# Performance work log

Hardware: AMD Instinct MI355X
Metric: run time of the kernel (lower is better)

Reference implementation:

```python
import jax, jax.numpy as jnp
import numpy as np

B, T, I, D = 64, 512, 512, 512


def hard_sigmoid(x):
    return jnp.clip(0.2 * x + 0.5, 0.0, 1.0)


def setup_inputs() -> dict:
    key = jax.random.key(0)
    ks = jax.random.split(key, 8)
    u = lambda k, sh: jax.random.uniform(k, sh, jnp.float32, -0.05, 0.05)  # keras 'uniform'
    gn = lambda k, sh: jax.random.normal(k, sh, jnp.float32) * jnp.sqrt(2.0 / (sh[0] + sh[1]))  # glorot_normal
    return {
        "X": jax.random.normal(ks[0], (B, T, I), jnp.float32),
        "W": u(ks[1], (I, D)),
        "b": jnp.zeros((D,), jnp.float32),
        "W_in": u(ks[2], (I, D)),
        "b_in": jnp.zeros((D,), jnp.float32),
        "W_out": u(ks[3], (I, D)),
        "b_out": jnp.zeros((D,), jnp.float32),
        "U": gn(ks[4], (D, D)),
        "U_in": gn(ks[5], (D, D)),
        "U_out": gn(ks[6], (D, D)),
        "bu_in": jnp.zeros((D,), jnp.float32),
        "bu_out": jnp.zeros((D,), jnp.float32),
    }


def reference(X, W, b, W_in, b_in, W_out, b_out, U, U_in, U_out, bu_in, bu_out):
    Xt = jnp.swapaxes(X, 0, 1)            # (T, B, I)
    xx = Xt @ W + b                       # (T, B, D) input projections (done once)
    x_in = Xt @ W_in + b_in
    x_out = Xt @ W_out + b_out
    # theano scan with sequence taps [-1,-2]: step t uses proj[t] and proj[t-1], t = 1..T-1
    seqs = (xx[1:], xx[:-1], x_in[1:], x_in[:-1], x_out[1:], x_out[:-1])

    def step(h, s):
        a, a_m1, p, p_m1, q, q_m1 = s
        z = hard_sigmoid(a + h @ U + a_m1)
        z_in = hard_sigmoid(p + h @ U_in + p_m1 + bu_in)
        z_out = jax.nn.softplus(q + (z_in * h) @ U_out + q_m1 + bu_out)
        h_t = (1.0 - z) * h + z * z_out
        return h_t, None

    h0 = jnp.zeros((X.shape[0], U.shape[0]), X.dtype)  # initial h_{-1} = 0
    h_last, _ = jax.lax.scan(step, h0, seqs)
    return h_last  # return_sequences=False -> last hidden state, (B, D)
```

## Files before the change

kernel.cpp:

```cpp
#include <hip/hip_runtime.h>
#include <hip/hip_bf16.h>


typedef __attribute__((ext_vector_type(4))) float  f32x4;
typedef __attribute__((ext_vector_type(4))) float  floatx4;
typedef __attribute__((ext_vector_type(8))) short  short8;
typedef __attribute__((ext_vector_type(4))) short  short4v;
typedef __attribute__((ext_vector_type(2))) int    int2v;

#define NSTEP  511
#define NGRP   4
#define NCOLB  32
#define NAN_S  ((short)0x7FFF)

#define OFF_HB0  4096
#define OFF_HB1  (OFF_HB0 + 65536)
#define OFF_GB0  (OFF_HB1 + 65536)
#define OFF_GB1  (OFF_GB0 + 65536)
#define OFF_HF32 (OFF_GB1 + 65536)
#define OFF_UPK  (OFF_HF32 + 131072)
#define OFF_WT   (OFF_UPK + 1572864)
#define OFF_XX   (OFF_WT + 1572864)
#define PER_T_BYTES (3u * 64u * 512u * 2u)

__device__ __forceinline__ float b2f(short s) {
  unsigned u = ((unsigned)(unsigned short)s) << 16;
  return __builtin_bit_cast(float, u);
}
__device__ __forceinline__ short f2b(float f) {
  unsigned u = __builtin_bit_cast(unsigned, f);
  u += 0x7fffu + ((u >> 16) & 1u);
  return (short)(u >> 16);
}
__device__ __forceinline__ float hsig(float x) {
  return fminf(fmaxf(0.2f * x + 0.5f, 0.0f), 1.0f);
}
__device__ __forceinline__ float softplus_f(float x) {
  return fmaxf(x, 0.0f) + log1pf(expf(-fabsf(x)));
}

__device__ __forceinline__ void st8_cp(short* p, int2v v) {
  asm volatile("global_store_dwordx2 %0, %1, off sc0 sc1"
               :: "v"(p), "v"(v) : "memory");
}

__device__ __forceinline__ void ld_frags16(const short* p0, const short* p1,
                                           const short* p2, const short* p3,
                                           short8 f[16]) {
  short8 f0,f1,f2,f3,f4,f5,f6,f7,f8,f9,f10,f11,f12,f13,f14,f15;
  asm volatile(
    "global_load_dwordx4 %0,  %16, off sc0 sc1\n\t"
    "global_load_dwordx4 %1,  %16, off offset:1024 sc0 sc1\n\t"
    "global_load_dwordx4 %2,  %16, off offset:2048 sc0 sc1\n\t"
    "global_load_dwordx4 %3,  %16, off offset:3072 sc0 sc1\n\t"
    "global_load_dwordx4 %4,  %17, off sc0 sc1\n\t"
    "global_load_dwordx4 %5,  %17, off offset:1024 sc0 sc1\n\t"
    "global_load_dwordx4 %6,  %17, off offset:2048 sc0 sc1\n\t"
    "global_load_dwordx4 %7,  %17, off offset:3072 sc0 sc1\n\t"
    "global_load_dwordx4 %8,  %18, off sc0 sc1\n\t"
    "global_load_dwordx4 %9,  %18, off offset:1024 sc0 sc1\n\t"
    "global_load_dwordx4 %10, %18, off offset:2048 sc0 sc1\n\t"
    "global_load_dwordx4 %11, %18, off offset:3072 sc0 sc1\n\t"
    "global_load_dwordx4 %12, %19, off sc0 sc1\n\t"
    "global_load_dwordx4 %13, %19, off offset:1024 sc0 sc1\n\t"
    "global_load_dwordx4 %14, %19, off offset:2048 sc0 sc1\n\t"
    "global_load_dwordx4 %15, %19, off offset:3072 sc0 sc1\n\t"
    "s_waitcnt vmcnt(0)"
    : "=&v"(f0), "=&v"(f1), "=&v"(f2), "=&v"(f3),
      "=&v"(f4), "=&v"(f5), "=&v"(f6), "=&v"(f7),
      "=&v"(f8), "=&v"(f9), "=&v"(f10), "=&v"(f11),
      "=&v"(f12), "=&v"(f13), "=&v"(f14), "=&v"(f15)
    : "v"(p0), "v"(p1), "v"(p2), "v"(p3)
    : "memory");
  f[0]=f0; f[1]=f1; f[2]=f2; f[3]=f3; f[4]=f4; f[5]=f5; f[6]=f6; f[7]=f7;
  f[8]=f8; f[9]=f9; f[10]=f10; f[11]=f11; f[12]=f12; f[13]=f13; f[14]=f14; f[15]=f15;
}

__device__ __forceinline__ void poll_frags16(const short* base, short8 f[16]) {
  const short* q0 = base;
  const short* q1 = base + 2048;
  const short* q2 = base + 4096;
  const short* q3 = base + 6144;
  int guard = 0;
  for (;;) {
    ld_frags16(q0, q1, q2, q3, f);
    int fresh = 1;
    #pragma unroll
    for (int i = 0; i < 16; ++i)
      fresh &= (f[i][0] != NAN_S) & (f[i][4] != NAN_S);
    if (__all(fresh)) break;
    if (++guard > (1 << 13)) break;
  }
}

__global__ __launch_bounds__(256) void prep_kernel(
    const float* __restrict__ U0, const float* __restrict__ U1, const float* __restrict__ U2,
    const float* __restrict__ W0, const float* __restrict__ W1, const float* __restrict__ W2,
    short* __restrict__ Upk, short* __restrict__ Wt)
{
  int e = blockIdx.x * 256 + threadIdx.x;
  if (e < 786432) {
    int mat = e >> 18;
    int rem = e & 262143;
    int c   = rem >> 13;
    int r2  = rem & 8191;
    int kb  = r2 >> 9;
    int r3  = r2 & 511;
    int l = r3 >> 3, j = r3 & 7;
    int k = kb * 32 + ((l >> 4) << 3) + j;
    int d = c * 16 + (l & 15);
    const float* U = (mat == 0) ? U0 : (mat == 1 ? U1 : U2);
    Upk[e] = f2b(U[k * 512 + d]);
  } else if (e < 1572864) {
    int e2 = e - 786432;
    int mat = e2 >> 18;
    int rem = e2 & 262143;
    int n = rem >> 9, k = rem & 511;
    const float* W = (mat == 0) ? W0 : (mat == 1 ? W1 : W2);
    Wt[e2] = f2b(W[k * 512 + n]);
  }
}

__global__ __launch_bounds__(256) void init_kernel(
    short* hb0, short* hb1, short* gb0, short* gb1, float* h_f32)
{
  int e = blockIdx.x * 256 + threadIdx.x;
  if (e < 32768) {
    hb0[e] = NAN_S; hb1[e] = 0;
    gb0[e] = NAN_S; gb1[e] = NAN_S;
    h_f32[e] = 0.0f;
  }
}

__global__ __launch_bounds__(256) void gemm_xw(
    const float* __restrict__ X, const short* __restrict__ Wt,
    const float* __restrict__ bias0, const float* __restrict__ bias1,
    const float* __restrict__ bias2, short* __restrict__ out,
    int base_row, int cnt_rows)
{
  __shared__ __align__(16) short Al[128][48];
  __shared__ __align__(16) short Bl[128][48];
  const int bm = blockIdx.x, bn = blockIdx.y, mat = blockIdx.z;
  const short* Wm = Wt + (size_t)mat * (512 * 512);
  const float* bias = (mat == 0) ? bias0 : (mat == 1 ? bias1 : bias2);
  short* om = out + (size_t)mat * ((size_t)cnt_rows * 512);
  const int tid = threadIdx.x, lane = tid & 63, wid = tid >> 6;
  const int wm = wid >> 1, wn = wid & 1;
  const int m0 = bm * 128, n0g = bn * 128;
  f32x4 acc[4][4];
  #pragma unroll
  for (int i = 0; i < 4; ++i)
    #pragma unroll
    for (int j = 0; j < 4; ++j) acc[i][j] = (f32x4){0.f, 0.f, 0.f, 0.f};

  for (int k0 = 0; k0 < 512; k0 += 32) {
    #pragma unroll
    for (int i = 0; i < 4; ++i) {
      int q = tid + 256 * i;
      int r = q >> 3, seg = q & 7;
      int ml = m0 + r;
      short4v h4 = {0, 0, 0, 0};
      if (ml < cnt_rows) {
        int gl = base_row + ml;
        int t = gl >> 6, bb = gl & 63;
        floatx4 v = *(const floatx4*)(X + ((size_t)bb * 512 + t) * 512 + k0 + seg * 4);
        h4 = (short4v){ f2b(v[0]), f2b(v[1]), f2b(v[2]), f2b(v[3]) };
      }
      *(short4v*)&Al[r][seg * 4] = h4;
    }
    #pragma unroll
    for (int i = 0; i < 2; ++i) {
      int q = tid + 256 * i;
      int r = q >> 2, seg = q & 3;
      *(short8*)&Bl[r][seg * 8] = *(const short8*)(Wm + (size_t)(n0g + r) * 512 + k0 + seg * 8);
    }
    __syncthreads();
    const int ko = (lane >> 4) * 8;
    short8 af[4], bf4[4];
    #pragma unroll
    for (int mt = 0; mt < 4; ++mt)
      af[mt] = *(const short8*)&Al[wm * 64 + mt * 16 + (lane & 15)][ko];
    #pragma unroll
    for (int nt = 0; nt < 4; ++nt)
      bf4[nt] = *(const short8*)&Bl[wn * 64 + nt * 16 + (lane & 15)][ko];
    #pragma unroll
    for (int mt = 0; mt < 4; ++mt)
      #pragma unroll
      for (int nt = 0; nt < 4; ++nt)
        acc[mt][nt] = __builtin_amdgcn_mfma_f32_16x16x32_bf16(af[mt], bf4[nt], acc[mt][nt], 0, 0, 0);
    __syncthreads();
  }
  const int rq = lane >> 4, cq = lane & 15;
  #pragma unroll
  for (int mt = 0; mt < 4; ++mt) {
    #pragma unroll
    for (int nt = 0; nt < 4; ++nt) {
      int n = n0g + wn * 64 + nt * 16 + cq;
      float bv = bias[n];
      #pragma unroll
      for (int rr = 0; rr < 4; ++rr) {
        int m = m0 + wm * 64 + mt * 16 + rq * 4 + rr;
        if (m < cnt_rows) om[(size_t)m * 512 + n] = f2b(acc[mt][nt][rr] + bv);
      }
    }
  }
}

__global__ __launch_bounds__(64, 1) void scan_kernel(
    short* hb0, short* hb1, short* gb0, short* gb1, float* h_f32,
    const short* __restrict__ Upk,
    const short* __restrict__ xx,
    const float* __restrict__ bu_in, const float* __restrict__ bu_out,
    float* __restrict__ out,
    int s0, int nsteps, int nt)
{
  __shared__ __align__(16) short Ub[3][16][64][8];
  __shared__ __align__(16) short St[256];
  const int lane = threadIdx.x & 63;
  const int g = blockIdx.x >> 5;
  const int c = blockIdx.x & 31;
  {
    const size_t cs = (size_t)c * 8192;
    short8* dst = (short8*)Ub;
    for (int i = lane; i < 3072; i += 64) {
      int mat = i >> 10;
      int rem = i & 1023;
      dst[i] = *(const short8*)(Upk + (size_t)mat * 262144 + cs + (size_t)rem * 8);
    }
  }
  const int colg = c * 16 + (lane & 15);
  const float binr  = bu_in[colg];
  const float boutr = bu_out[colg];
  const size_t XSZ = (size_t)nt * 64 * 512;
  const int gbase = g * 8192;
  const int fofs = gbase + ((lane >> 4) << 7) + ((lane & 15) << 3);
  const int pofs = gbase + ((c >> 1) << 9) + ((c & 1) << 8) + (lane << 2);
  const int sw = ((lane & 15) >> 3) * 128 + ((lane >> 4) << 5) + (lane & 7);
  short* hbuf[2] = { hb0, hb1 };
  short* gbuf[2] = { gb0, gb1 };
  const int2v NANPAIR = { 0x7FFF7FFF, 0x7FFF7FFF };

  float hown[4];
  #pragma unroll
  for (int r = 0; r < 4; ++r)
    hown[r] = h_f32[(size_t)(g * 16 + (lane >> 4) * 4 + r) * 512 + colg];
  __syncthreads();

  for (int s = 0; s < nsteps; ++s) {
    const int sg = s0 + s;
    const int p = sg & 1;
    float a1[4], a0[4], p1[4], p0[4], q1[4], q0[4];
    #pragma unroll
    for (int r = 0; r < 4; ++r) {
      int gr = g * 16 + (lane >> 4) * 4 + r;
      size_t i1 = ((size_t)(s + 1) * 64 + gr) * 512 + colg;
      size_t i0 = ((size_t)s * 64 + gr) * 512 + colg;
      a1[r] = b2f(xx[i1]);           a0[r] = b2f(xx[i0]);
      p1[r] = b2f(xx[XSZ + i1]);     p0[r] = b2f(xx[XSZ + i0]);
      q1[r] = b2f(xx[2 * XSZ + i1]); q0[r] = b2f(xx[2 * XSZ + i0]);
    }

    short8 afr[16];
    poll_frags16(hbuf[p ^ 1] + fofs, afr);
    if (sg > 0) st8_cp(gbuf[p ^ 1] + pofs, NANPAIR);

    f32x4 ai[4];
    ai[0] = ai[1] = ai[2] = ai[3] = (f32x4){0.f, 0.f, 0.f, 0.f};
    #pragma unroll
    for (int kb = 0; kb < 16; ++kb) {
      short8 b1 = *((const short8*)Ub + ((1 * 16 + kb) * 64 + lane));
      ai[kb & 3] = __builtin_amdgcn_mfma_f32_16x16x32_bf16(afr[kb], b1, ai[kb & 3], 0, 0, 0);
    }
    f32x4 accin = (ai[0] + ai[1]) + (ai[2] + ai[3]);
    #pragma unroll
    for (int r = 0; r < 4; ++r) {
      float zin = hsig(p1[r] + accin[r] + p0[r] + binr);
      St[sw + r * 8] = f2b(zin * hown[r]);
    }
    st8_cp(gbuf[p] + pofs, *(const int2v*)&St[lane << 2]);

    f32x4 au[4];
    au[0] = au[1] = au[2] = au[3] = (f32x4){0.f, 0.f, 0.f, 0.f};
    #pragma unroll
    for (int kb = 0; kb < 16; ++kb) {
      short8 b0 = *((const short8*)Ub + ((0 * 16 + kb) * 64 + lane));
      au[kb & 3] = __builtin_amdgcn_mfma_f32_16x16x32_bf16(afr[kb], b0, au[kb & 3], 0, 0, 0);
    }
    f32x4 accu = (au[0] + au[1]) + (au[2] + au[3]);
    float zr[4];
    #pragma unroll
    for (int r = 0; r < 4; ++r)
      zr[r] = hsig(a1[r] + accu[r] + a0[r]);

    short8 gfr[16];
    poll_frags16(gbuf[p] + fofs, gfr);
    st8_cp(hbuf[p ^ 1] + pofs, NANPAIR);
    f32x4 ao[4];
    ao[0] = ao[1] = ao[2] = ao[3] = (f32x4){0.f, 0.f, 0.f, 0.f};
    #pragma unroll
    for (int kb = 0; kb < 16; ++kb) {
      short8 b2 = *((const short8*)Ub + ((2 * 16 + kb) * 64 + lane));
      ao[kb & 3] = __builtin_amdgcn_mfma_f32_16x16x32_bf16(gfr[kb], b2, ao[kb & 3], 0, 0, 0);
    }
    f32x4 acco = (ao[0] + ao[1]) + (ao[2] + ao[3]);
    #pragma unroll
    for (int r = 0; r < 4; ++r) {
      float pre = q1[r] + acco[r] + q0[r] + boutr;
      float zo = softplus_f(pre);
      float hn = (1.0f - zr[r]) * hown[r] + zr[r] * zo;
      hown[r] = hn;
      St[sw + r * 8] = f2b(hn);
    }
    st8_cp(hbuf[p] + pofs, *(const int2v*)&St[lane << 2]);
    if (sg == NSTEP - 1) {
      #pragma unroll
      for (int r = 0; r < 4; ++r) {
        int gr = g * 16 + (lane >> 4) * 4 + r;
        out[(size_t)gr * 512 + colg] = hown[r];
      }
    }
  }
  #pragma unroll
  for (int r = 0; r < 4; ++r)
    h_f32[(size_t)(g * 16 + (lane >> 4) * 4 + r) * 512 + colg] = hown[r];
  asm volatile("s_waitcnt vmcnt(0)" ::: "memory");
}

extern "C" void kernel_launch(void* const* d_in, const int* in_sizes, int n_in,
                              void* d_out, int out_size, void* d_ws, size_t ws_size,
                              hipStream_t stream)
{
  const float* X      = (const float*)d_in[0];
  const float* W      = (const float*)d_in[1];
  const float* b      = (const float*)d_in[2];
  const float* W_in   = (const float*)d_in[3];
  const float* b_in   = (const float*)d_in[4];
  const float* W_out  = (const float*)d_in[5];
  const float* b_out  = (const float*)d_in[6];
  const float* U      = (const float*)d_in[7];
  const float* U_in   = (const float*)d_in[8];
  const float* U_out  = (const float*)d_in[9];
  const float* bu_in  = (const float*)d_in[10];
  const float* bu_out = (const float*)d_in[11];
  float* out = (float*)d_out;
  char* ws = (char*)d_ws;
  short* hb0  = (short*)(ws + OFF_HB0);
  short* hb1  = (short*)(ws + OFF_HB1);
  short* gb0  = (short*)(ws + OFF_GB0);
  short* gb1  = (short*)(ws + OFF_GB1);
  float* h_f32= (float*)(ws + OFF_HF32);
  short* Upk  = (short*)(ws + OFF_UPK);
  short* Wt   = (short*)(ws + OFF_WT);
  short* xx   = (short*)(ws + OFF_XX);

  size_t avail = (ws_size > (size_t)OFF_XX) ? ws_size - (size_t)OFF_XX : 0;
  int max_t = (int)(avail / PER_T_BYTES);
  if (max_t > 512) max_t = 512;
  int SEG = max_t - 1;
  if (SEG < 1) SEG = 1;

  prep_kernel<<<6144, 256, 0, stream>>>(U, U_in, U_out, W, W_in, W_out, Upk, Wt);
  init_kernel<<<128, 256, 0, stream>>>(hb0, hb1, gb0, gb1, h_f32);

  int s0 = 0;
  while (s0 < NSTEP) {
    int nsteps = NSTEP - s0; if (nsteps > SEG) nsteps = SEG;
    int nt = nsteps + 1;
    int rows = nt * 64;
    int gx = (rows + 127) / 128;
    gemm_xw<<<dim3(gx, 4, 3), 256, 0, stream>>>(X, Wt, b, b_in, b_out, xx,
                                                s0 * 64, rows);
    scan_kernel<<<NGRP * NCOLB, 64, 0, stream>>>(hb0, hb1, gb0, gb1, h_f32,
                                                 Upk, xx, bu_in, bu_out, out,
                                                 s0, nsteps, nt);
    s0 += nsteps;
  }
}
```

Measured before the change: 2.657 ms.

## Consume fresh h/g fragments incrementally while double-buffered polls stay in flight

Replaces the all-or-nothing polling loop, which waited until all 16 fragments were non-NaN before any MFMA, with a per-fragment freshness mask. Each fragment is fed into the MFMAs as soon as it is seen to be fresh, while the next poll load is already issued into a second register buffer. The U and U_in products are also fused into one pass over the h fragments. The aim is to overlap the cross-block synchronisation latency with matrix work, at the cost of many more registers, branchy code and a possibly different accumulation order.

```diff
diff --git a/kernel.cpp b/kernel.cpp
--- a/kernel.cpp
+++ b/kernel.cpp
@@ -44,10 +44,13 @@
                :: "v"(p), "v"(v) : "memory");
 }
 
-__device__ __forceinline__ void ld_frags16(const short* p0, const short* p1,
+struct Frags {
+  short8 f0,f1,f2,f3,f4,f5,f6,f7,f8,f9,f10,f11,f12,f13,f14,f15;
+};
+
+__device__ __forceinline__ void ld_issue16(const short* p0, const short* p1,
                                            const short* p2, const short* p3,
-                                           short8 f[16]) {
-  short8 f0,f1,f2,f3,f4,f5,f6,f7,f8,f9,f10,f11,f12,f13,f14,f15;
+                                           Frags& F) {
   asm volatile(
     "global_load_dwordx4 %0,  %16, off sc0 sc1\n\t"
     "global_load_dwordx4 %1,  %16, off offset:1024 sc0 sc1\n\t"
@@ -64,34 +67,65 @@
     "global_load_dwordx4 %12, %19, off sc0 sc1\n\t"
     "global_load_dwordx4 %13, %19, off offset:1024 sc0 sc1\n\t"
     "global_load_dwordx4 %14, %19, off offset:2048 sc0 sc1\n\t"
-    "global_load_dwordx4 %15, %19, off offset:3072 sc0 sc1\n\t"
-    "s_waitcnt vmcnt(0)"
-    : "=&v"(f0), "=&v"(f1), "=&v"(f2), "=&v"(f3),
-      "=&v"(f4), "=&v"(f5), "=&v"(f6), "=&v"(f7),
-      "=&v"(f8), "=&v"(f9), "=&v"(f10), "=&v"(f11),
-      "=&v"(f12), "=&v"(f13), "=&v"(f14), "=&v"(f15)
+    "global_load_dwordx4 %15, %19, off offset:3072 sc0 sc1"
+    : "=&v"(F.f0), "=&v"(F.f1), "=&v"(F.f2), "=&v"(F.f3),
+      "=&v"(F.f4), "=&v"(F.f5), "=&v"(F.f6), "=&v"(F.f7),
+      "=&v"(F.f8), "=&v"(F.f9), "=&v"(F.f10), "=&v"(F.f11),
+      "=&v"(F.f12), "=&v"(F.f13), "=&v"(F.f14), "=&v"(F.f15)
     : "v"(p0), "v"(p1), "v"(p2), "v"(p3)
     : "memory");
-  f[0]=f0; f[1]=f1; f[2]=f2; f[3]=f3; f[4]=f4; f[5]=f5; f[6]=f6; f[7]=f7;
-  f[8]=f8; f[9]=f9; f[10]=f10; f[11]=f11; f[12]=f12; f[13]=f13; f[14]=f14; f[15]=f15;
-}
-
-__device__ __forceinline__ void poll_frags16(const short* base, short8 f[16]) {
-  const short* q0 = base;
-  const short* q1 = base + 2048;
-  const short* q2 = base + 4096;
-  const short* q3 = base + 6144;
-  int guard = 0;
-  for (;;) {
-    ld_frags16(q0, q1, q2, q3, f);
-    int fresh = 1;
-    #pragma unroll
-    for (int i = 0; i < 16; ++i)
-      fresh &= (f[i][0] != NAN_S) & (f[i][4] != NAN_S);
-    if (__all(fresh)) break;
-    if (++guard > (1 << 13)) break;
-  }
-}
+}
+
+__device__ __forceinline__ void vmw(Frags& F) {
+  asm volatile("s_waitcnt vmcnt(0)"
+    : "+v"(F.f0), "+v"(F.f1), "+v"(F.f2), "+v"(F.f3),
+      "+v"(F.f4), "+v"(F.f5), "+v"(F.f6), "+v"(F.f7),
+      "+v"(F.f8), "+v"(F.f9), "+v"(F.f10), "+v"(F.f11),
+      "+v"(F.f12), "+v"(F.f13), "+v"(F.f14), "+v"(F.f15)
+    :: "memory");
+}
+
+#define FRESHBIT(F, i) \
+  (((unsigned)__all(((F).f##i[0] != NAN_S) & ((F).f##i[4] != NAN_S))) << i)
+
+__device__ __forceinline__ unsigned freshmask_impl(const Frags& F) {
+  unsigned m = 0;
+  m |= FRESHBIT(F, 0);  m |= FRESHBIT(F, 1);  m |= FRESHBIT(F, 2);
+  m |= FRESHBIT(F, 3);  m |= FRESHBIT(F, 4);  m |= FRESHBIT(F, 5);
+  m |= FRESHBIT(F, 6);  m |= FRESHBIT(F, 7);  m |= FRESHBIT(F, 8);
+  m |= FRESHBIT(F, 9);  m |= FRESHBIT(F, 10); m |= FRESHBIT(F, 11);
+  m |= FRESHBIT(F, 12); m |= FRESHBIT(F, 13); m |= FRESHBIT(F, 14);
+  m |= FRESHBIT(F, 15);
+  return m;
+}
+
+#define MF(a, b, c) __builtin_amdgcn_mfma_f32_16x16x32_bf16(a, b, c, 0, 0, 0)
+
+#define CONS1_ONE(F, i) \
+  if ((fr >> i) & 1) { \
+    short8 b0 = *((const short8*)Ub + ((0 * 16 + i) * 64 + lane)); \
+    short8 b1 = *((const short8*)Ub + ((1 * 16 + i) * 64 + lane)); \
+    au[i & 3] = MF((F).f##i, b0, au[i & 3]); \
+    ai[i & 3] = MF((F).f##i, b1, ai[i & 3]); \
+  }
+#define CONS1_ALL(F) do { \
+  CONS1_ONE(F, 0)  CONS1_ONE(F, 1)  CONS1_ONE(F, 2)  CONS1_ONE(F, 3)  \
+  CONS1_ONE(F, 4)  CONS1_ONE(F, 5)  CONS1_ONE(F, 6)  CONS1_ONE(F, 7)  \
+  CONS1_ONE(F, 8)  CONS1_ONE(F, 9)  CONS1_ONE(F, 10) CONS1_ONE(F, 11) \
+  CONS1_ONE(F, 12) CONS1_ONE(F, 13) CONS1_ONE(F, 14) CONS1_ONE(F, 15) \
+} while (0)
+
+#define CONS2_ONE(F, i) \
+  if ((fr >> i) & 1) { \
+    short8 b2 = *((const short8*)Ub + ((2 * 16 + i) * 64 + lane)); \
+    ao[i & 3] = MF((F).f##i, b2, ao[i & 3]); \
+  }
+#define CONS2_ALL(F) do { \
+  CONS2_ONE(F, 0)  CONS2_ONE(F, 1)  CONS2_ONE(F, 2)  CONS2_ONE(F, 3)  \
+  CONS2_ONE(F, 4)  CONS2_ONE(F, 5)  CONS2_ONE(F, 6)  CONS2_ONE(F, 7)  \
+  CONS2_ONE(F, 8)  CONS2_ONE(F, 9)  CONS2_ONE(F, 10) CONS2_ONE(F, 11) \
+  CONS2_ONE(F, 12) CONS2_ONE(F, 13) CONS2_ONE(F, 14) CONS2_ONE(F, 15) \
+} while (0)
 
 __global__ __launch_bounds__(256) void prep_kernel(
     const float* __restrict__ U0, const float* __restrict__ U1, const float* __restrict__ U2,
@@ -246,6 +280,8 @@
     hown[r] = h_f32[(size_t)(g * 16 + (lane >> 4) * 4 + r) * 512 + colg];
   __syncthreads();
 
+  Frags FA, FB;
+
   for (int s = 0; s < nsteps; ++s) {
     const int sg = s0 + s;
     const int p = sg & 1;
@@ -260,17 +296,33 @@
       q1[r] = b2f(xx[2 * XSZ + i1]); q0[r] = b2f(xx[2 * XSZ + i0]);
     }
 
-    short8 afr[16];
-    poll_frags16(hbuf[p ^ 1] + fofs, afr);
+    const short* hbp = hbuf[p ^ 1] + fofs;
+    f32x4 au[4], ai[4];
+    au[0] = au[1] = au[2] = au[3] = (f32x4){0.f, 0.f, 0.f, 0.f};
+    ai[0] = ai[1] = ai[2] = ai[3] = (f32x4){0.f, 0.f, 0.f, 0.f};
+    {
+      unsigned done = 0; int guard = 0;
+      ld_issue16(hbp, hbp + 2048, hbp + 4096, hbp + 6144, FA);
+      for (;;) {
+        vmw(FA);
+        unsigned fr = freshmask_impl(FA) & ~done;
+        unsigned nd = done | fr;
+        if (nd != 0xFFFFu) ld_issue16(hbp, hbp + 2048, hbp + 4096, hbp + 6144, FB);
+        CONS1_ALL(FA);
+        done = nd;
+        if (done == 0xFFFFu) break;
+        if (++guard > 4096) break;
+        vmw(FB);
+        fr = freshmask_impl(FB) & ~done;
+        nd = done | fr;
+        if (nd != 0xFFFFu) ld_issue16(hbp, hbp + 2048, hbp + 4096, hbp + 6144, FA);
+        CONS1_ALL(FB);
+        done = nd;
+        if (done == 0xFFFFu) break;
+        if (++guard > 4096) break;
+      }
+    }
     if (sg > 0) st8_cp(gbuf[p ^ 1] + pofs, NANPAIR);
-
-    f32x4 ai[4];
-    ai[0] = ai[1] = ai[2] = ai[3] = (f32x4){0.f, 0.f, 0.f, 0.f};
-    #pragma unroll
-    for (int kb = 0; kb < 16; ++kb) {
-      short8 b1 = *((const short8*)Ub + ((1 * 16 + kb) * 64 + lane));
-      ai[kb & 3] = __builtin_amdgcn_mfma_f32_16x16x32_bf16(afr[kb], b1, ai[kb & 3], 0, 0, 0);
-    }
     f32x4 accin = (ai[0] + ai[1]) + (ai[2] + ai[3]);
     #pragma unroll
     for (int r = 0; r < 4; ++r) {
@@ -278,30 +330,38 @@
       St[sw + r * 8] = f2b(zin * hown[r]);
     }
     st8_cp(gbuf[p] + pofs, *(const int2v*)&St[lane << 2]);
-
-    f32x4 au[4];
-    au[0] = au[1] = au[2] = au[3] = (f32x4){0.f, 0.f, 0.f, 0.f};
-    #pragma unroll
-    for (int kb = 0; kb < 16; ++kb) {
-      short8 b0 = *((const short8*)Ub + ((0 * 16 + kb) * 64 + lane));
-      au[kb & 3] = __builtin_amdgcn_mfma_f32_16x16x32_bf16(afr[kb], b0, au[kb & 3], 0, 0, 0);
-    }
     f32x4 accu = (au[0] + au[1]) + (au[2] + au[3]);
     float zr[4];
     #pragma unroll
     for (int r = 0; r < 4; ++r)
       zr[r] = hsig(a1[r] + accu[r] + a0[r]);
 
-    short8 gfr[16];
-    poll_frags16(gbuf[p] + fofs, gfr);
-    st8_cp(hbuf[p ^ 1] + pofs, NANPAIR);
+    const short* gbp = gbuf[p] + fofs;
     f32x4 ao[4];
     ao[0] = ao[1] = ao[2] = ao[3] = (f32x4){0.f, 0.f, 0.f, 0.f};
-    #pragma unroll
-    for (int kb = 0; kb < 16; ++kb) {
-      short8 b2 = *((const short8*)Ub + ((2 * 16 + kb) * 64 + lane));
-      ao[kb & 3] = __builtin_amdgcn_mfma_f32_16x16x32_bf16(gfr[kb], b2, ao[kb & 3], 0, 0, 0);
-    }
+    {
+      unsigned done = 0; int guard = 0;
+      ld_issue16(gbp, gbp + 2048, gbp + 4096, gbp + 6144, FA);
+      for (;;) {
+        vmw(FA);
+        unsigned fr = freshmask_impl(FA) & ~done;
+        unsigned nd = done | fr;
+        if (nd != 0xFFFFu) ld_issue16(gbp, gbp + 2048, gbp + 4096, gbp + 6144, FB);
+        CONS2_ALL(FA);
+        done = nd;
+        if (done == 0xFFFFu) break;
+        if (++guard > 4096) break;
+        vmw(FB);
+        fr = freshmask_impl(FB) & ~done;
+        nd = done | fr;
+        if (nd != 0xFFFFu) ld_issue16(gbp, gbp + 2048, gbp + 4096, gbp + 6144, FA);
+        CONS2_ALL(FB);
+        done = nd;
+        if (done == 0xFFFFu) break;
+        if (++guard > 4096) break;
+      }
+    }
+    st8_cp(hbuf[p ^ 1] + pofs, NANPAIR);
     f32x4 acco = (ao[0] + ao[1]) + (ao[2] + ao[3]);
     #pragma unroll
     for (int r = 0; r < 4; ++r) {
```

New measurement: 3.528 ms. 1.33x slower.
